# Optimization experiments

Measured on AMD Instinct MI355X. Metric: run time of the kernel, lower is better.

## Reference

```python
import jax, jax.numpy as jnp
import numpy as np

D, NH, DH = 1024, 16, 64
QLEN, MLEN, B = 1024, 1024, 2
KLEN = QLEN + MLEN
RLEN = KLEN + QLEN
EPS = 1e-12
SCALE = 1.0 / (DH ** 0.5)
STD = 0.02


def setup_inputs() -> dict:
    key = jax.random.key(0)
    ks = jax.random.split(key, 14)
    h = jax.random.normal(ks[0], (QLEN, B, D), jnp.float32)
    mems = jax.random.normal(ks[1], (MLEN, B, D), jnp.float32)
    r = jax.random.normal(ks[2], (RLEN, B, D), jnp.float32)
    # segment ids -> one-hot same/diff segment matrix [q, k, b, 2]
    seg_q = jax.random.randint(ks[3], (QLEN, B), 0, 2)
    seg_k = jax.random.randint(ks[4], (KLEN, B), 0, 2)
    diff = (seg_q[:, None, :] != seg_k[None, :, :]).astype(jnp.int32)
    seg_mat = jax.nn.one_hot(diff, 2, dtype=jnp.float32)
    attn_mask = (jax.random.uniform(ks[5], (QLEN, KLEN, B, 1)) < 0.1).astype(jnp.float32)
    q_w = STD * jax.random.normal(ks[6], (D, NH, DH), jnp.float32)
    k_w = STD * jax.random.normal(ks[7], (D, NH, DH), jnp.float32)
    v_w = STD * jax.random.normal(ks[8], (D, NH, DH), jnp.float32)
    o_w = STD * jax.random.normal(ks[9], (D, NH, DH), jnp.float32)
    r_w = STD * jax.random.normal(ks[10], (D, NH, DH), jnp.float32)
    r_w_bias = jnp.zeros((NH, DH), jnp.float32)
    r_r_bias = jnp.zeros((NH, DH), jnp.float32)
    r_s_bias = jnp.zeros((NH, DH), jnp.float32)
    seg_embed = STD * jax.random.normal(ks[11], (2, NH, DH), jnp.float32)
    ln_gamma = jnp.ones((D,), jnp.float32)
    ln_beta = jnp.zeros((D,), jnp.float32)
    return dict(h=h, mems=mems, r=r, seg_mat=seg_mat, attn_mask=attn_mask,
                q_w=q_w, k_w=k_w, v_w=v_w, o_w=o_w, r_w=r_w,
                r_w_bias=r_w_bias, r_r_bias=r_r_bias, r_s_bias=r_s_bias,
                seg_embed=seg_embed, ln_gamma=ln_gamma, ln_beta=ln_beta)


def rel_shift(x, klen):
    # x: [qlen, rlen, b, n] -> [qlen, klen, b, n]
    q, rl, b, n = x.shape
    x = x.reshape(rl, q, b, n)[1:]
    return x.reshape(q, rl - 1, b, n)[:, :klen]


def reference(h, mems, r, seg_mat, attn_mask, q_w, k_w, v_w, o_w, r_w,
              r_w_bias, r_r_bias, r_s_bias, seg_embed, ln_gamma, ln_beta):
    cat = jnp.concatenate([mems, h], axis=0)          # [klen, b, D]
    q_head = jnp.einsum('ibh,hnd->ibnd', h, q_w)      # [q, b, n, d]
    k_head = jnp.einsum('ibh,hnd->ibnd', cat, k_w)    # [k, b, n, d]
    v_head = jnp.einsum('ibh,hnd->ibnd', cat, v_w)
    k_r = jnp.einsum('ibh,hnd->ibnd', r, r_w)         # [rlen, b, n, d]
    # content term
    ac = jnp.einsum('ibnd,jbnd->ijbn', q_head + r_w_bias, k_head)
    # position term with relative shift
    bd = jnp.einsum('ibnd,jbnd->ijbn', q_head + r_r_bias, k_r)
    bd = rel_shift(bd, ac.shape[1])
    # segment term
    ef = jnp.einsum('ibnd,snd->ibns', q_head + r_s_bias, seg_embed)
    ef = jnp.einsum('ijbs,ibns->ijbn', seg_mat, ef)
    attn_score = (ac + bd + ef) * SCALE - 1e30 * attn_mask
    attn_prob = jax.nn.softmax(attn_score, axis=1)
    attn_vec = jnp.einsum('ijbn,jbnd->ibnd', attn_prob, v_head)
    attn_out = jnp.einsum('ibnd,hnd->ibh', attn_vec, o_w) + h  # residual
    mu = jnp.mean(attn_out, axis=-1, keepdims=True)
    var = jnp.var(attn_out, axis=-1, keepdims=True)
    return (attn_out - mu) * jax.lax.rsqrt(var + EPS) * ln_gamma + ln_beta
```

## Files before the change

kernel.cpp:

```cpp
#include <hip/hip_runtime.h>
#include <hip/hip_fp16.h>

#define QLEN 1024
#define MLEN 1024
#define KLEN 2048
#define RLEN 3072
#define BB 2
#define NH 16
#define DHH 64
#define DD 1024
#define SCALE 0.125f

typedef float f32x4 __attribute__((ext_vector_type(4)));
typedef short bfx8 __attribute__((ext_vector_type(8)));

__device__ __forceinline__ unsigned short f2bf(float f) {
    unsigned int u = __float_as_uint(f);
    unsigned int lsb = (u >> 16) & 1u;
    u += 0x7fffu + lsb;
    return (unsigned short)(u >> 16);
}

__global__ __launch_bounds__(256) void k_pack(const float* __restrict__ seg,
                                              const float* __restrict__ msk,
                                              unsigned char* __restrict__ flags) {
    const int idx = blockIdx.x * 256 + threadIdx.x;
    const float diff = seg[(size_t)idx * 2 + 1];
    const float mk = msk[idx];
    flags[idx] = (unsigned char)((diff > 0.5f ? 1 : 0) | (mk > 0.5f ? 2 : 0));
}

__global__ __launch_bounds__(256) void k_cvt_all(
    const float* __restrict__ h, const float* __restrict__ mems,
    const float* __restrict__ r, const float* __restrict__ ow,
    unsigned short* __restrict__ hb, unsigned short* __restrict__ mb,
    unsigned short* __restrict__ rb, unsigned short* __restrict__ owb) {
    const int blk = blockIdx.x;
    const float* src; unsigned short* dst; int base;
    if (blk < 1024)      { src = h;    dst = hb;  base = blk; }
    else if (blk < 2048) { src = mems; dst = mb;  base = blk - 1024; }
    else if (blk < 5120) { src = r;    dst = rb;  base = blk - 2048; }
    else                 { src = ow;   dst = owb; base = blk - 5120; }
    const size_t idx = ((size_t)base * 256 + threadIdx.x) * 8;
    float4 v0 = *(const float4*)&src[idx];
    float4 v1 = *(const float4*)&src[idx + 4];
    bfx8 o;
    o[0] = (short)f2bf(v0.x); o[1] = (short)f2bf(v0.y);
    o[2] = (short)f2bf(v0.z); o[3] = (short)f2bf(v0.w);
    o[4] = (short)f2bf(v1.x); o[5] = (short)f2bf(v1.y);
    o[6] = (short)f2bf(v1.z); o[7] = (short)f2bf(v1.w);
    *(bfx8*)&dst[idx] = o;
}

__global__ __launch_bounds__(256) void k_cvtT(
    const float* __restrict__ w0, const float* __restrict__ w1,
    const float* __restrict__ w2, const float* __restrict__ w3,
    unsigned short* __restrict__ o0, unsigned short* __restrict__ o1,
    unsigned short* __restrict__ o2, unsigned short* __restrict__ o3) {
    __shared__ float Ts[64][65];
    const float* W; unsigned short* Wb;
    switch (blockIdx.z) {
        case 0:  W = w0; Wb = o0; break;
        case 1:  W = w1; Wb = o1; break;
        case 2:  W = w2; Wb = o2; break;
        default: W = w3; Wb = o3; break;
    }
    const int k0 = blockIdx.x * 64, n0 = blockIdx.y * 64;
    const int t = threadIdx.x;
#pragma unroll
    for (int e = 0; e < 4; e++) {
        int row = e * 16 + (t >> 4), col = (t & 15) * 4;
        *(float4*)&Ts[row][col] = *(const float4*)&W[(size_t)(k0 + row) * 1024 + n0 + col];
    }
    __syncthreads();
    const int n_l = t >> 2, kc = (t & 3) * 16;
    bfx8 a, b;
#pragma unroll
    for (int i = 0; i < 8; i++) a[i] = (short)f2bf(Ts[kc + i][n_l]);
#pragma unroll
    for (int i = 0; i < 8; i++) b[i] = (short)f2bf(Ts[kc + 8 + i][n_l]);
    unsigned short* dst = &Wb[(size_t)(n0 + n_l) * 1024 + k0 + kc];
    *(bfx8*)dst = a;
    *(bfx8*)(dst + 8) = b;
}

template <int MODE>
__global__ __launch_bounds__(256) void k_gemm(
    const unsigned short* __restrict__ A0, const unsigned short* __restrict__ A1,
    const int split, const int rowstride, const int bstride,
    const unsigned short* __restrict__ Bm, const float* __restrict__ res,
    float* __restrict__ outp, const int R) {
    __shared__ __align__(16) unsigned short As[128 * 32];
    __shared__ __align__(16) unsigned short Bs[128 * 32];
    const int t = threadIdx.x;
    const int wave = t >> 6, lane = t & 63;
    const int r0 = blockIdx.x * 128, c0 = blockIdx.y * 128;
    const int b = blockIdx.z;
    const int wr = (wave >> 1) * 64, wc = (wave & 1) * 64;
    const int bofs = b * bstride;

    f32x4 acc[4][4];
#pragma unroll
    for (int m = 0; m < 4; m++)
#pragma unroll
        for (int n = 0; n < 4; n++) acc[m][n] = (f32x4)0.f;

    const int srow = t >> 2;
    const int skc = (t & 3) * 8;
    const unsigned short* arow[2];
    const unsigned short* brow[2];
#pragma unroll
    for (int e = 0; e < 2; e++) {
        int rg = r0 + srow + e * 64;
        arow[e] = ((rg < split) ? (A0 + (size_t)rg * rowstride)
                                : (A1 + (size_t)(rg - split) * rowstride)) + bofs;
        brow[e] = Bm + (size_t)(c0 + srow + e * 64) * 1024;
    }

    const int l15 = lane & 15, kc8 = (lane >> 4) * 8;
    for (int k0 = 0; k0 < 1024; k0 += 32) {
#pragma unroll
        for (int e = 0; e < 2; e++) {
            *(bfx8*)&As[(srow + e * 64) * 32 + skc] = *(const bfx8*)(arow[e] + k0 + skc);
            *(bfx8*)&Bs[(srow + e * 64) * 32 + skc] = *(const bfx8*)(brow[e] + k0 + skc);
        }
        __syncthreads();
        bfx8 af[4], bfr[4];
#pragma unroll
        for (int m = 0; m < 4; m++)
            af[m] = *(const bfx8*)&As[(wr + m * 16 + l15) * 32 + kc8];
#pragma unroll
        for (int n = 0; n < 4; n++)
            bfr[n] = *(const bfx8*)&Bs[(wc + n * 16 + l15) * 32 + kc8];
#pragma unroll
        for (int m = 0; m < 4; m++)
#pragma unroll
            for (int n = 0; n < 4; n++)
                acc[m][n] = __builtin_amdgcn_mfma_f32_16x16x32_bf16(
                    af[m], bfr[n], acc[m][n], 0, 0, 0);
        __syncthreads();
    }

    const int rq = (lane >> 4) * 4;
#pragma unroll
    for (int m = 0; m < 4; m++) {
#pragma unroll
        for (int n = 0; n < 4; n++) {
            const int colg = c0 + wc + n * 16 + l15;
            if (MODE == 0 || MODE == 2) {
                const int head = colg >> 6, dh = colg & 63;
                const size_t ob = ((size_t)(b * 16 + head) * R) * 64 + dh;
#pragma unroll
                for (int q = 0; q < 4; q++) {
                    const int rowg = r0 + wr + m * 16 + rq + q;
                    if (MODE == 0)
                        outp[ob + (size_t)rowg * 64] = acc[m][n][q];
                    else
                        ((unsigned short*)outp)[ob + (size_t)rowg * 64] = f2bf(acc[m][n][q]);
                }
            } else {
#pragma unroll
                for (int q = 0; q < 4; q++) {
                    const int rowg = r0 + wr + m * 16 + rq + q;
                    const size_t o = (size_t)rowg * 1024 + colg;
                    outp[o] = acc[m][n][q] + res[o];
                }
            }
        }
    }
}

__global__ __launch_bounds__(256) void k_scorepv_mfma(
    const float* __restrict__ qh, const unsigned short* __restrict__ khb,
    const unsigned short* __restrict__ vhb, const unsigned short* __restrict__ krhb,
    const unsigned char* __restrict__ flags, const float* __restrict__ rw_bias,
    const float* __restrict__ rr_bias, const float* __restrict__ rs_bias,
    const float* __restrict__ seg_embed, unsigned short* __restrict__ avb) {
    __shared__ __align__(16) unsigned short qcs[64][72];
    __shared__ __align__(16) unsigned short qrs[64][72];
    __shared__ __align__(16) unsigned short ks[64][72];
    __shared__ __align__(16) unsigned short vts[64][72];
    __shared__ __align__(16) unsigned short krs[2][64][72];
    __shared__ __align__(16) unsigned short pws[4][16][72];
    __shared__ float efs[64][2];

    const int itile = blockIdx.x, bn = blockIdx.y;
    const int b = bn >> 4, n = bn & 15;
    const int i0 = itile * 64;
    const int t = threadIdx.x;
    const int lane = t & 63, wave = t >> 6;
    const int l15 = lane & 15, kc8 = (lane >> 4) * 8;
    const int srow = t >> 2, sdb = (t & 3) * 16;

    {
        const float* qp = &qh[((size_t)bn * QLEN + i0 + srow) * DHH + sdb];
#pragma unroll
        for (int e = 0; e < 4; e++) {
            float4 qv = *(const float4*)&qp[e * 4];
            float4 bw = *(const float4*)&rw_bias[n * DHH + sdb + e * 4];
            float4 br = *(const float4*)&rr_bias[n * DHH + sdb + e * 4];
            short4 c, r;
            c.x = (short)f2bf(qv.x + bw.x); c.y = (short)f2bf(qv.y + bw.y);
            c.z = (short)f2bf(qv.z + bw.z); c.w = (short)f2bf(qv.w + bw.w);
            r.x = (short)f2bf(qv.x + br.x); r.y = (short)f2bf(qv.y + br.y);
            r.z = (short)f2bf(qv.z + br.z); r.w = (short)f2bf(qv.w + br.w);
            *(short4*)&qcs[srow][sdb + e * 4] = c;
            *(short4*)&qrs[srow][sdb + e * 4] = r;
        }
    }
    if (t < 128) {
        int i = t >> 1, s = t & 1;
        float sum = 0.f;
        for (int d = 0; d < DHH; d++) {
            float qraw = qh[((size_t)bn * QLEN + i0 + i) * DHH + d] + rs_bias[n * DHH + d];
            sum += qraw * seg_embed[(s * NH + n) * DHH + d];
        }
        efs[i][s] = sum;
    }
    __syncthreads();

    bfx8 qcf[2], qrf[2];
#pragma unroll
    for (int kk = 0; kk < 2; kk++) {
        qcf[kk] = *(const bfx8*)&qcs[wave * 16 + l15][kk * 32 + kc8];
        qrf[kk] = *(const bfx8*)&qrs[wave * 16 + l15][kk * 32 + kc8];
    }

    f32x4 acc[4];
#pragma unroll
    for (int nf = 0; nf < 4; nf++) acc[nf] = (f32x4)0.f;
    float m_r[4], l_r[4];
#pragma unroll
    for (int q = 0; q < 4; q++) { m_r[q] = -3.0e38f; l_r[q] = 0.f; }

    const int v0w = 48 - wave * 16;
    const int rowl = (lane >> 4) * 4;

    for (int jt = 0; jt < 32; jt++) {
        const int j0 = jt * 64;
        const int jrlo = QLEN + j0 - i0 - 63;
        __syncthreads();
        {
            const unsigned short* kp = &khb[((size_t)bn * KLEN + j0 + srow) * DHH + sdb];
            *(bfx8*)&ks[srow][sdb] = *(const bfx8*)kp;
            *(bfx8*)&ks[srow][sdb + 8] = *(const bfx8*)(kp + 8);
        }
        {
            const unsigned short* vp = &vhb[((size_t)bn * KLEN + j0 + srow) * DHH + sdb];
            bfx8 v0 = *(const bfx8*)vp;
            bfx8 v1 = *(const bfx8*)(vp + 8);
#pragma unroll
            for (int e = 0; e < 8; e++) vts[sdb + e][srow] = (unsigned short)v0[e];
#pragma unroll
            for (int e = 0; e < 8; e++) vts[sdb + 8 + e][srow] = (unsigned short)v1[e];
        }
        {
            int jr = jrlo + 64 + srow;
            if (jr > RLEN - 1) jr = RLEN - 1;
            const unsigned short* krp = &krhb[((size_t)bn * RLEN + jr) * DHH + sdb];
            unsigned short* dst = &krs[(jt + 1) & 1][srow][sdb];
            *(bfx8*)dst = *(const bfx8*)krp;
            *(bfx8*)(dst + 8) = *(const bfx8*)(krp + 8);
            if (jt == 0) {
                int jr0 = jrlo + srow;
                const unsigned short* krp0 = &krhb[((size_t)bn * RLEN + jr0) * DHH + sdb];
                unsigned short* dst0 = &krs[0][srow][sdb];
                *(bfx8*)dst0 = *(const bfx8*)krp0;
                *(bfx8*)(dst0 + 8) = *(const bfx8*)(krp0 + 8);
            }
        }
        __syncthreads();

        f32x4 acF[4];
#pragma unroll
        for (int nf = 0; nf < 4; nf++) {
            f32x4 a = (f32x4)0.f;
#pragma unroll
            for (int kk = 0; kk < 2; kk++) {
                bfx8 kf = *(const bfx8*)&ks[nf * 16 + l15][kk * 32 + kc8];
                a = __builtin_amdgcn_mfma_f32_16x16x32_bf16(qcf[kk], kf, a, 0, 0, 0);
            }
            acF[nf] = a;
        }
        f32x4 bF[5];
#pragma unroll
        for (int f = 0; f < 5; f++) {
            const int v = v0w + f * 16;
            const int bi = (jt + (v >> 6)) & 1;
            const int vr = v & 63;
            f32x4 a = (f32x4)0.f;
#pragma unroll
            for (int kk = 0; kk < 2; kk++) {
                bfx8 kf = *(const bfx8*)&krs[bi][vr + l15][kk * 32 + kc8];
                a = __builtin_amdgcn_mfma_f32_16x16x32_bf16(qrf[kk], kf, a, 0, 0, 0);
            }
            bF[f] = a;
        }

        float p[4][4];
#pragma unroll
        for (int nf = 0; nf < 4; nf++) {
#pragma unroll
            for (int q = 0; q < 4; q++) {
                const int row = rowl + q;
                const int src = (lane & 48) | ((15 - row + l15) & 15);
                float ba = __shfl(bF[nf][q], src);
                float bb = __shfl(bF[nf + 1][q], src);
                float bd = (l15 > row) ? bb : ba;
                const int gi = i0 + wave * 16 + row;
                const int gj = j0 + nf * 16 + l15;
                const unsigned char fl = flags[((size_t)gi * KLEN + gj) * BB + b];
                float sc = (acF[nf][q] + bd + efs[wave * 16 + row][fl & 1]) * SCALE;
                if (fl & 2) sc -= 1e30f;
                p[nf][q] = sc;
            }
        }

        float corr[4];
#pragma unroll
        for (int q = 0; q < 4; q++) {
            float mx = fmaxf(fmaxf(p[0][q], p[1][q]), fmaxf(p[2][q], p[3][q]));
            mx = fmaxf(mx, __shfl_xor(mx, 1));
            mx = fmaxf(mx, __shfl_xor(mx, 2));
            mx = fmaxf(mx, __shfl_xor(mx, 4));
            mx = fmaxf(mx, __shfl_xor(mx, 8));
            const float mnew = fmaxf(m_r[q], mx);
            corr[q] = __expf(m_r[q] - mnew);
            float ps = 0.f;
#pragma unroll
            for (int nf = 0; nf < 4; nf++) {
                float e = __expf(p[nf][q] - mnew);
                p[nf][q] = e;
                ps += e;
            }
            ps += __shfl_xor(ps, 1);
            ps += __shfl_xor(ps, 2);
            ps += __shfl_xor(ps, 4);
            ps += __shfl_xor(ps, 8);
            l_r[q] = l_r[q] * corr[q] + ps;
            m_r[q] = mnew;
        }
#pragma unroll
        for (int nf = 0; nf < 4; nf++)
#pragma unroll
            for (int q = 0; q < 4; q++) acc[nf][q] *= corr[q];
#pragma unroll
        for (int nf = 0; nf < 4; nf++)
#pragma unroll
            for (int q = 0; q < 4; q++)
                pws[wave][rowl + q][nf * 16 + l15] = f2bf(p[nf][q]);
        bfx8 pa[2];
#pragma unroll
        for (int kk = 0; kk < 2; kk++)
            pa[kk] = *(const bfx8*)&pws[wave][l15][kk * 32 + kc8];
#pragma unroll
        for (int nf = 0; nf < 4; nf++) {
#pragma unroll
            for (int kk = 0; kk < 2; kk++) {
                bfx8 vf = *(const bfx8*)&vts[nf * 16 + l15][kk * 32 + kc8];
                acc[nf] = __builtin_amdgcn_mfma_f32_16x16x32_bf16(pa[kk], vf, acc[nf], 0, 0, 0);
            }
        }
    }

#pragma unroll
    for (int q = 0; q < 4; q++) {
        const float inv = 1.f / l_r[q];
        const int gi = i0 + wave * 16 + rowl + q;
#pragma unroll
        for (int nf = 0; nf < 4; nf++)
            avb[((size_t)gi * BB + b) * DD + n * DHH + nf * 16 + l15] =
                f2bf(acc[nf][q] * inv);
    }
}

__global__ __launch_bounds__(256) void k_ln(const float* __restrict__ ao,
                                            const float* __restrict__ gamma,
                                            const float* __restrict__ beta,
                                            float* __restrict__ outp) {
    const int row = blockIdx.x;
    const int t = threadIdx.x;
    float4 x = *(const float4*)&ao[(size_t)row * DD + t * 4];
    float s = x.x + x.y + x.z + x.w;
    float ss = x.x * x.x + x.y * x.y + x.z * x.z + x.w * x.w;
#pragma unroll
    for (int o = 1; o < 64; o <<= 1) {
        s += __shfl_xor(s, o);
        ss += __shfl_xor(ss, o);
    }
    __shared__ float sbuf[4], ssbuf[4];
    const int w = t >> 6;
    if ((t & 63) == 0) {
        sbuf[w] = s;
        ssbuf[w] = ss;
    }
    __syncthreads();
    s = sbuf[0] + sbuf[1] + sbuf[2] + sbuf[3];
    ss = ssbuf[0] + ssbuf[1] + ssbuf[2] + ssbuf[3];
    const float mu = s * (1.f / 1024.f);
    const float var = ss * (1.f / 1024.f) - mu * mu;
    const float rs = rsqrtf(var + 1e-12f);
    float4 g = *(const float4*)&gamma[t * 4];
    float4 bt = *(const float4*)&beta[t * 4];
    float4 o4;
    o4.x = (x.x - mu) * rs * g.x + bt.x;
    o4.y = (x.y - mu) * rs * g.y + bt.y;
    o4.z = (x.z - mu) * rs * g.z + bt.z;
    o4.w = (x.w - mu) * rs * g.w + bt.w;
    *(float4*)&outp[(size_t)row * DD + t * 4] = o4;
}

extern "C" void kernel_launch(void* const* d_in, const int* in_sizes, int n_in,
                              void* d_out, int out_size, void* d_ws, size_t ws_size,
                              hipStream_t stream) {
    (void)in_sizes; (void)n_in; (void)out_size; (void)ws_size;
    const float* h        = (const float*)d_in[0];
    const float* mems     = (const float*)d_in[1];
    const float* r        = (const float*)d_in[2];
    const float* seg_mat  = (const float*)d_in[3];
    const float* attn_mask= (const float*)d_in[4];
    const float* q_w      = (const float*)d_in[5];
    const float* k_w      = (const float*)d_in[6];
    const float* v_w      = (const float*)d_in[7];
    const float* o_w      = (const float*)d_in[8];
    const float* r_w      = (const float*)d_in[9];
    const float* r_w_bias = (const float*)d_in[10];
    const float* r_r_bias = (const float*)d_in[11];
    const float* r_s_bias = (const float*)d_in[12];
    const float* seg_embed= (const float*)d_in[13];
    const float* ln_gamma = (const float*)d_in[14];
    const float* ln_beta  = (const float*)d_in[15];
    float* outp = (float*)d_out;

    char* w = (char*)d_ws;
    unsigned short* hb  = (unsigned short*)w; w += (size_t)2097152 * 2;
    unsigned short* mb  = (unsigned short*)w; w += (size_t)2097152 * 2;
    unsigned short* rb  = (unsigned short*)w; w += (size_t)6291456 * 2;
    unsigned short* owb = (unsigned short*)w; w += (size_t)1048576 * 2;
    unsigned short* qwb = (unsigned short*)w; w += (size_t)1048576 * 2;
    unsigned short* kwb = (unsigned short*)w; w += (size_t)1048576 * 2;
    unsigned short* vwb = (unsigned short*)w; w += (size_t)1048576 * 2;
    unsigned short* rwb = (unsigned short*)w; w += (size_t)1048576 * 2;
    float* qh = (float*)w;           w += (size_t)BB * NH * QLEN * DHH * 4;
    unsigned short* khb  = (unsigned short*)w; w += (size_t)BB * NH * KLEN * DHH * 2;
    unsigned short* vhb  = (unsigned short*)w; w += (size_t)BB * NH * KLEN * DHH * 2;
    unsigned short* krhb = (unsigned short*)w; w += (size_t)BB * NH * RLEN * DHH * 2;
    unsigned short* avb = (unsigned short*)w; w += (size_t)2097152 * 2;
    unsigned char* flags = (unsigned char*)w; w += (size_t)QLEN * KLEN * BB;
    float* ao = qh;

    k_pack<<<(QLEN * KLEN * BB) / 256, 256, 0, stream>>>(seg_mat, attn_mask, flags);
    k_cvt_all<<<5632, 256, 0, stream>>>(h, mems, r, o_w, hb, mb, rb, owb);
    k_cvtT<<<dim3(16, 16, 4), 256, 0, stream>>>(q_w, k_w, v_w, r_w, qwb, kwb, vwb, rwb);

    k_gemm<0><<<dim3(8, 8, 2), 256, 0, stream>>>(hb, hb, 1024, 2048, 1024, qwb,
                                                 nullptr, qh, QLEN);
    k_gemm<2><<<dim3(16, 8, 2), 256, 0, stream>>>(mb, hb, 1024, 2048, 1024, kwb,
                                                  nullptr, (float*)khb, KLEN);
    k_gemm<2><<<dim3(16, 8, 2), 256, 0, stream>>>(mb, hb, 1024, 2048, 1024, vwb,
                                                  nullptr, (float*)vhb, KLEN);
    k_gemm<2><<<dim3(24, 8, 2), 256, 0, stream>>>(rb, rb, 3072, 2048, 1024, rwb,
                                                  nullptr, (float*)krhb, RLEN);

    k_scorepv_mfma<<<dim3(16, 32), 256, 0, stream>>>(qh, khb, vhb, krhb, flags,
                                                     r_w_bias, r_r_bias, r_s_bias,
                                                     seg_embed, avb);

    k_gemm<1><<<dim3(16, 8, 1), 256, 0, stream>>>(avb, avb, 2048, 1024, 0, owb,
                                                  h, ao, 0);

    k_ln<<<QLEN * BB, 256, 0, stream>>>(ao, ln_gamma, ln_beta, outp);
}
```

Baseline: 414.0 us.

## Store V transposed from GEMM, split flags per batch, alias shared memory buffers

The V projection GEMM gets a new epilogue mode that writes V head-transposed ([b,n,d,k]) in bf16, so the attention kernel loads V tiles with vector copies instead of an 8-way scalar transpose into shared memory. The packed mask/segment flags are laid out per batch so each block reads contiguous bytes rather than stride-2 bytes. Shared memory buffers are aliased (Q tiles reused for V^T and P scratch) to cut LDS footprint and possibly raise occupancy. The GEMM epilogue now does strided short4 stores, which may write less efficiently.

```diff
diff --git a/kernel.cpp b/kernel.cpp
--- a/kernel.cpp
+++ b/kernel.cpp
@@ -10,6 +10,7 @@
 #define DHH 64
 #define DD 1024
 #define SCALE 0.125f
+#define QK ((size_t)QLEN * KLEN)
 
 typedef float f32x4 __attribute__((ext_vector_type(4)));
 typedef short bfx8 __attribute__((ext_vector_type(8)));
@@ -23,11 +24,12 @@
 
 __global__ __launch_bounds__(256) void k_pack(const float* __restrict__ seg,
                                               const float* __restrict__ msk,
-                                              unsigned char* __restrict__ flags) {
+                                              unsigned char* __restrict__ flagsP) {
     const int idx = blockIdx.x * 256 + threadIdx.x;
     const float diff = seg[(size_t)idx * 2 + 1];
     const float mk = msk[idx];
-    flags[idx] = (unsigned char)((diff > 0.5f ? 1 : 0) | (mk > 0.5f ? 2 : 0));
+    flagsP[(size_t)(idx & 1) * QK + (idx >> 1)] =
+        (unsigned char)((diff > 0.5f ? 1 : 0) | (mk > 0.5f ? 2 : 0));
 }
 
 __global__ __launch_bounds__(256) void k_cvt_all(
@@ -147,8 +149,8 @@
 #pragma unroll
         for (int n = 0; n < 4; n++) {
             const int colg = c0 + wc + n * 16 + l15;
+            const int head = colg >> 6, dh = colg & 63;
             if (MODE == 0 || MODE == 2) {
-                const int head = colg >> 6, dh = colg & 63;
                 const size_t ob = ((size_t)(b * 16 + head) * R) * 64 + dh;
 #pragma unroll
                 for (int q = 0; q < 4; q++) {
@@ -158,6 +160,15 @@
                     else
                         ((unsigned short*)outp)[ob + (size_t)rowg * 64] = f2bf(acc[m][n][q]);
                 }
+            } else if (MODE == 3) {
+                const size_t ob = ((size_t)(b * 16 + head) * 64 + dh) * R +
+                                  (r0 + wr + m * 16 + rq);
+                short4 o;
+                o.x = (short)f2bf(acc[m][n][0]);
+                o.y = (short)f2bf(acc[m][n][1]);
+                o.z = (short)f2bf(acc[m][n][2]);
+                o.w = (short)f2bf(acc[m][n][3]);
+                *(short4*)&((unsigned short*)outp)[ob] = o;
             } else {
 #pragma unroll
                 for (int q = 0; q < 4; q++) {
@@ -172,17 +183,16 @@
 
 __global__ __launch_bounds__(256) void k_scorepv_mfma(
     const float* __restrict__ qh, const unsigned short* __restrict__ khb,
-    const unsigned short* __restrict__ vhb, const unsigned short* __restrict__ krhb,
-    const unsigned char* __restrict__ flags, const float* __restrict__ rw_bias,
+    const unsigned short* __restrict__ vhT, const unsigned short* __restrict__ krhb,
+    const unsigned char* __restrict__ flagsP, const float* __restrict__ rw_bias,
     const float* __restrict__ rr_bias, const float* __restrict__ rs_bias,
     const float* __restrict__ seg_embed, unsigned short* __restrict__ avb) {
-    __shared__ __align__(16) unsigned short qcs[64][72];
-    __shared__ __align__(16) unsigned short qrs[64][72];
-    __shared__ __align__(16) unsigned short ks[64][72];
-    __shared__ __align__(16) unsigned short vts[64][72];
-    __shared__ __align__(16) unsigned short krs[2][64][72];
-    __shared__ __align__(16) unsigned short pws[4][16][72];
+    __shared__ __align__(16) unsigned short smem[23040];
     __shared__ float efs[64][2];
+    unsigned short (*qcs)[72] = (unsigned short(*)[72])smem;
+    unsigned short (*vts)[72] = (unsigned short(*)[72])smem;
+    unsigned short (*qrs)[72] = (unsigned short(*)[72])(smem + 4608);
+    unsigned short (*ks)[72]  = (unsigned short(*)[72])(smem + 9216);
 
     const int itile = blockIdx.x, bn = blockIdx.y;
     const int b = bn >> 4, n = bn & 15;
@@ -191,6 +201,7 @@
     const int lane = t & 63, wave = t >> 6;
     const int l15 = lane & 15, kc8 = (lane >> 4) * 8;
     const int srow = t >> 2, sdb = (t & 3) * 16;
+    unsigned short (*pws)[72] = (unsigned short(*)[72])(smem + 4608 + wave * 16 * 72);
 
     {
         const float* qp = &qh[((size_t)bn * QLEN + i0 + srow) * DHH + sdb];
@@ -235,6 +246,7 @@
 
     const int v0w = 48 - wave * 16;
     const int rowl = (lane >> 4) * 4;
+    const unsigned char* flb = &flagsP[(size_t)b * QK];
 
     for (int jt = 0; jt < 32; jt++) {
         const int j0 = jt * 64;
@@ -246,25 +258,21 @@
             *(bfx8*)&ks[srow][sdb + 8] = *(const bfx8*)(kp + 8);
         }
         {
-            const unsigned short* vp = &vhb[((size_t)bn * KLEN + j0 + srow) * DHH + sdb];
-            bfx8 v0 = *(const bfx8*)vp;
-            bfx8 v1 = *(const bfx8*)(vp + 8);
-#pragma unroll
-            for (int e = 0; e < 8; e++) vts[sdb + e][srow] = (unsigned short)v0[e];
-#pragma unroll
-            for (int e = 0; e < 8; e++) vts[sdb + 8 + e][srow] = (unsigned short)v1[e];
+            const unsigned short* vp = &vhT[((size_t)bn * 64 + srow) * KLEN + j0 + sdb];
+            *(bfx8*)&vts[srow][sdb] = *(const bfx8*)vp;
+            *(bfx8*)&vts[srow][sdb + 8] = *(const bfx8*)(vp + 8);
         }
         {
             int jr = jrlo + 64 + srow;
             if (jr > RLEN - 1) jr = RLEN - 1;
             const unsigned short* krp = &krhb[((size_t)bn * RLEN + jr) * DHH + sdb];
-            unsigned short* dst = &krs[(jt + 1) & 1][srow][sdb];
+            unsigned short* dst = &smem[13824 + (((jt + 1) & 1) * 64 + srow) * 72 + sdb];
             *(bfx8*)dst = *(const bfx8*)krp;
             *(bfx8*)(dst + 8) = *(const bfx8*)(krp + 8);
             if (jt == 0) {
                 int jr0 = jrlo + srow;
                 const unsigned short* krp0 = &krhb[((size_t)bn * RLEN + jr0) * DHH + sdb];
-                unsigned short* dst0 = &krs[0][srow][sdb];
+                unsigned short* dst0 = &smem[13824 + srow * 72 + sdb];
                 *(bfx8*)dst0 = *(const bfx8*)krp0;
                 *(bfx8*)(dst0 + 8) = *(const bfx8*)(krp0 + 8);
             }
@@ -291,7 +299,7 @@
             f32x4 a = (f32x4)0.f;
 #pragma unroll
             for (int kk = 0; kk < 2; kk++) {
-                bfx8 kf = *(const bfx8*)&krs[bi][vr + l15][kk * 32 + kc8];
+                bfx8 kf = *(const bfx8*)&smem[13824 + (bi * 64 + vr + l15) * 72 + kk * 32 + kc8];
                 a = __builtin_amdgcn_mfma_f32_16x16x32_bf16(qrf[kk], kf, a, 0, 0, 0);
             }
             bF[f] = a;
@@ -309,7 +317,7 @@
                 float bd = (l15 > row) ? bb : ba;
                 const int gi = i0 + wave * 16 + row;
                 const int gj = j0 + nf * 16 + l15;
-                const unsigned char fl = flags[((size_t)gi * KLEN + gj) * BB + b];
+                const unsigned char fl = flb[(size_t)gi * KLEN + gj];
                 float sc = (acF[nf][q] + bd + efs[wave * 16 + row][fl & 1]) * SCALE;
                 if (fl & 2) sc -= 1e30f;
                 p[nf][q] = sc;
@@ -348,11 +356,11 @@
         for (int nf = 0; nf < 4; nf++)
 #pragma unroll
             for (int q = 0; q < 4; q++)
-                pws[wave][rowl + q][nf * 16 + l15] = f2bf(p[nf][q]);
+                pws[rowl + q][nf * 16 + l15] = f2bf(p[nf][q]);
         bfx8 pa[2];
 #pragma unroll
         for (int kk = 0; kk < 2; kk++)
-            pa[kk] = *(const bfx8*)&pws[wave][l15][kk * 32 + kc8];
+            pa[kk] = *(const bfx8*)&pws[l15][kk * 32 + kc8];
 #pragma unroll
         for (int nf = 0; nf < 4; nf++) {
 #pragma unroll
@@ -443,13 +451,13 @@
     unsigned short* rwb = (unsigned short*)w; w += (size_t)1048576 * 2;
     float* qh = (float*)w;           w += (size_t)BB * NH * QLEN * DHH * 4;
     unsigned short* khb  = (unsigned short*)w; w += (size_t)BB * NH * KLEN * DHH * 2;
-    unsigned short* vhb  = (unsigned short*)w; w += (size_t)BB * NH * KLEN * DHH * 2;
+    unsigned short* vhT  = (unsigned short*)w; w += (size_t)BB * NH * KLEN * DHH * 2;
     unsigned short* krhb = (unsigned short*)w; w += (size_t)BB * NH * RLEN * DHH * 2;
     unsigned short* avb = (unsigned short*)w; w += (size_t)2097152 * 2;
-    unsigned char* flags = (unsigned char*)w; w += (size_t)QLEN * KLEN * BB;
+    unsigned char* flagsP = (unsigned char*)w; w += QK * BB;
     float* ao = qh;
 
-    k_pack<<<(QLEN * KLEN * BB) / 256, 256, 0, stream>>>(seg_mat, attn_mask, flags);
+    k_pack<<<(QLEN * KLEN * BB) / 256, 256, 0, stream>>>(seg_mat, attn_mask, flagsP);
     k_cvt_all<<<5632, 256, 0, stream>>>(h, mems, r, o_w, hb, mb, rb, owb);
     k_cvtT<<<dim3(16, 16, 4), 256, 0, stream>>>(q_w, k_w, v_w, r_w, qwb, kwb, vwb, rwb);
 
@@ -457,12 +465,12 @@
                                                  nullptr, qh, QLEN);
     k_gemm<2><<<dim3(16, 8, 2), 256, 0, stream>>>(mb, hb, 1024, 2048, 1024, kwb,
                                                   nullptr, (float*)khb, KLEN);
-    k_gemm<2><<<dim3(16, 8, 2), 256, 0, stream>>>(mb, hb, 1024, 2048, 1024, vwb,
-                                                  nullptr, (float*)vhb, KLEN);
+    k_gemm<3><<<dim3(16, 8, 2), 256, 0, stream>>>(mb, hb, 1024, 2048, 1024, vwb,
+                                                  nullptr, (float*)vhT, KLEN);
     k_gemm<2><<<dim3(24, 8, 2), 256, 0, stream>>>(rb, rb, 3072, 2048, 1024, rwb,
                                                   nullptr, (float*)krhb, RLEN);
 
-    k_scorepv_mfma<<<dim3(16, 32), 256, 0, stream>>>(qh, khb, vhb, krhb, flags,
+    k_scorepv_mfma<<<dim3(16, 32), 256, 0, stream>>>(qh, khb, vhT, krhb, flagsP,
                                                      r_w_bias, r_r_bias, r_s_bias,
                                                      seg_embed, avb);
 
```

New measurement: 458.5 us. 10.8% more time.
